# Optimization experiments

Hardware: AMD Instinct MI355X
Metric: run time of the kernel (lower is better)

The kernel has to match this reference:

```python
import jax, jax.numpy as jnp
import numpy as np

COUT, CIN = 1024, 1024  # self.shape = (cout, cin) in the torch module
NNZ = 131072


def setup_inputs() -> dict:
    key = jax.random.key(0)
    k_x, k_v, k_r, k_c = jax.random.split(key, 4)
    x = jax.random.normal(k_x, (4, 4096, CIN), dtype=jnp.float32)
    values = jax.random.normal(k_v, (NNZ,), dtype=jnp.float32)
    rows = jax.random.randint(k_r, (NNZ,), 0, COUT, dtype=jnp.int32)
    cols = jax.random.randint(k_c, (NNZ,), 0, CIN, dtype=jnp.int32)
    indices = jnp.stack([rows, cols], axis=0)  # [2, nnz], integer-valued
    return {"x": x, "values": values, "indices": indices}


def reference(x, values, indices):
    # torch: sparse_coo_tensor(indices, values, (cout, cin)).coalesce();
    # coalescing sums duplicate (row, col) entries -> scatter-add densify.
    rows, cols = indices[0], indices[1]
    W = jnp.zeros((COUT, CIN), dtype=values.dtype).at[rows, cols].add(values)
    # 3D path: out[b, l, co] = sum_ci W[co, ci] * x[b, l, ci]
    return jnp.einsum('blc,oc->blo', x, W)
```

## Files before the change

### kernel.cpp

```cpp
#include <hip/hip_runtime.h>
#include <cstdint>
#include <cstddef>

#define CIN  1024
#define COUT 1024

typedef __attribute__((ext_vector_type(8))) short bf16x8;
typedef __attribute__((ext_vector_type(4))) float f32x4;

__device__ __forceinline__ unsigned short f2bf(float f) {
    union { float f; unsigned int i; } v;
    v.f = f;
    unsigned int u = v.i;
    u += 0x7FFFu + ((u >> 16) & 1u);
    return (unsigned short)(u >> 16);
}

__global__ void zero_f32(float4* __restrict__ p) {
    p[blockIdx.x * 256 + threadIdx.x] = float4{0.f, 0.f, 0.f, 0.f};
}

__global__ void scatter_add(const float* __restrict__ vals,
                            const int* __restrict__ rows,
                            const int* __restrict__ cols,
                            float* __restrict__ W, int nnz) {
    int i = blockIdx.x * 256 + threadIdx.x;
    if (i < nnz) {
        atomicAdd(W + (size_t)rows[i] * CIN + cols[i], vals[i]);
    }
}

__global__ void cvt_bf16_bulk(const float* __restrict__ src, unsigned short* __restrict__ dst) {
    size_t i = ((size_t)blockIdx.x * 256 + threadIdx.x) * 8;
    float4 v0 = *(const float4*)(src + i);
    float4 v1 = *(const float4*)(src + i + 4);
    union { bf16x8 v; unsigned short u[8]; } w;
    w.u[0] = f2bf(v0.x); w.u[1] = f2bf(v0.y); w.u[2] = f2bf(v0.z); w.u[3] = f2bf(v0.w);
    w.u[4] = f2bf(v1.x); w.u[5] = f2bf(v1.y); w.u[6] = f2bf(v1.z); w.u[7] = f2bf(v1.w);
    *(bf16x8*)(dst + i) = w.v;
}

__global__ __launch_bounds__(256) void gemm_bt_bf16_sw(
    const unsigned short* __restrict__ A,
    const unsigned short* __restrict__ B,
    float* __restrict__ C,
    int M) {
    constexpr int K = CIN;
    constexpr int N = COUT;

    __shared__ __align__(16) unsigned short As[128 * 64];
    __shared__ __align__(16) unsigned short Bs[128 * 64];

    const int tid   = threadIdx.x;
    const int lane  = tid & 63;
    const int wave  = tid >> 6;
    const int waveM = (wave >> 1) * 64;
    const int waveN = (wave & 1) * 64;
    const int quad  = lane >> 4;
    const int l16   = lane & 15;

    const int rowA0 = blockIdx.x * 128;
    const int rowB0 = blockIdx.y * 128;

    const int stg_r  = tid >> 3;
    const int c_slot = tid & 7;
    const int c_data = c_slot ^ (stg_r & 7);
    const unsigned short* pa = A + (size_t)(rowA0 + stg_r) * K + c_data * 8;
    const unsigned short* pb = B + (size_t)(rowB0 + stg_r) * K + c_data * 8;
    const int ldsoff = tid * 8;

    f32x4 acc[4][4] = {};

    for (int k0 = 0; k0 < K; k0 += 64) {
#pragma unroll
        for (int it = 0; it < 4; ++it) {
            __builtin_amdgcn_global_load_lds(
                (const __attribute__((address_space(1))) void*)(pa + k0 + (size_t)it * 32 * K),
                (__attribute__((address_space(3))) void*)(As + it * 2048 + ldsoff),
                16, 0, 0);
            __builtin_amdgcn_global_load_lds(
                (const __attribute__((address_space(1))) void*)(pb + k0 + (size_t)it * 32 * K),
                (__attribute__((address_space(3))) void*)(Bs + it * 2048 + ldsoff),
                16, 0, 0);
        }
        __syncthreads();

        const int s7 = l16 & 7;
#pragma unroll
        for (int ks = 0; ks < 2; ++ks) {
            bf16x8 af[4], bfr[4];
            const int cx = ((ks * 4 + quad) ^ s7) * 8;
#pragma unroll
            for (int t = 0; t < 4; ++t) {
                af[t]  = *(const bf16x8*)(As + (waveM + t * 16 + l16) * 64 + cx);
                bfr[t] = *(const bf16x8*)(Bs + (waveN + t * 16 + l16) * 64 + cx);
            }
#pragma unroll
            for (int i = 0; i < 4; ++i)
#pragma unroll
                for (int j = 0; j < 4; ++j)
                    acc[i][j] = __builtin_amdgcn_mfma_f32_16x16x32_bf16(
                        af[i], bfr[j], acc[i][j], 0, 0, 0);
        }
        __syncthreads();
    }

#pragma unroll
    for (int i = 0; i < 4; ++i) {
#pragma unroll
        for (int r = 0; r < 4; ++r) {
            const int row = rowA0 + waveM + i * 16 + quad * 4 + r;
            float* cp = C + (size_t)row * N + rowB0 + waveN + l16;
#pragma unroll
            for (int j = 0; j < 4; ++j)
                cp[j * 16] = acc[i][j][r];
        }
    }
}

extern "C" void kernel_launch(void* const* d_in, const int* in_sizes, int n_in,
                              void* d_out, int out_size, void* d_ws, size_t ws_size,
                              hipStream_t stream) {
    const float* x    = (const float*)d_in[0];
    const float* vals = (const float*)d_in[1];
    const int*   idx  = (const int*)d_in[2];

    float* out = (float*)d_out;

    const int nnz = in_sizes[2] / 2;
    const int M   = in_sizes[0] / CIN;

    const size_t wf_bytes = (size_t)COUT * CIN * sizeof(float);
    const size_t wb_bytes = (size_t)COUT * CIN * sizeof(unsigned short);

    float*          Wf = (float*)d_ws;
    unsigned short* Wb = (unsigned short*)((char*)d_ws + wf_bytes);
    unsigned short* Xb = (unsigned short*)((char*)d_ws + wf_bytes + wb_bytes);

    zero_f32<<<dim3(COUT * CIN / (256 * 4)), dim3(256), 0, stream>>>((float4*)Wf);
    scatter_add<<<dim3((nnz + 255) / 256), dim3(256), 0, stream>>>(vals, idx, idx + nnz, Wf, nnz);
    cvt_bf16_bulk<<<dim3(COUT * CIN / (256 * 8)), dim3(256), 0, stream>>>(Wf, Wb);
    cvt_bf16_bulk<<<dim3((unsigned)((size_t)M * CIN / (256 * 8))), dim3(256), 0, stream>>>(x, Xb);
    gemm_bt_bf16_sw<<<dim3(M / 128, COUT / 128), dim3(256), 0, stream>>>(Xb, Wb, out, M);
}
```

Measured before the change: 163.8 us.

## Load A fragments directly from global memory and stage larger B tiles in LDS

The GEMM stops staging the activation tile in shared memory and has each lane read its bf16 A fragments straight from global memory. The weight tile is staged in LDS in 256-wide K chunks, which cuts the number of barrier-separated iterations from sixteen to four. The aim is to remove the A LDS traffic and the barrier overhead. In exchange it adds uncoalesced global loads, duplicate A reads across waves, and 64KB of LDS per block, which may lower occupancy.

```diff
diff --git a/kernel.cpp b/kernel.cpp
--- a/kernel.cpp
+++ b/kernel.cpp
@@ -40,7 +40,7 @@
     *(bf16x8*)(dst + i) = w.v;
 }
 
-__global__ __launch_bounds__(256) void gemm_bt_bf16_sw(
+__global__ __launch_bounds__(256) void gemm_adirect(
     const unsigned short* __restrict__ A,
     const unsigned short* __restrict__ B,
     float* __restrict__ C,
@@ -48,8 +48,7 @@
     constexpr int K = CIN;
     constexpr int N = COUT;
 
-    __shared__ __align__(16) unsigned short As[128 * 64];
-    __shared__ __align__(16) unsigned short Bs[128 * 64];
+    __shared__ __align__(16) unsigned short Bs[128 * 256];
 
     const int tid   = threadIdx.x;
     const int lane  = tid & 63;
@@ -62,47 +61,48 @@
     const int rowA0 = blockIdx.x * 128;
     const int rowB0 = blockIdx.y * 128;
 
-    const int stg_r  = tid >> 3;
-    const int c_slot = tid & 7;
-    const int c_data = c_slot ^ (stg_r & 7);
-    const unsigned short* pa = A + (size_t)(rowA0 + stg_r) * K + c_data * 8;
-    const unsigned short* pb = B + (size_t)(rowB0 + stg_r) * K + c_data * 8;
+    const int s_slot = tid & 31;
+    const int r_low  = tid >> 5;
+    const int c_data = (s_slot & ~7) | ((s_slot & 7) ^ r_low);
+    const unsigned short* pb = B + (size_t)(rowB0 + r_low) * K + c_data * 8;
     const int ldsoff = tid * 8;
 
+    const unsigned short* pa = A + (size_t)(rowA0 + waveM + l16) * K + quad * 8;
+
     f32x4 acc[4][4] = {};
+    const int s7 = l16 & 7;
 
-    for (int k0 = 0; k0 < K; k0 += 64) {
+    for (int kq = 0; kq < 4; ++kq) {
+        if (kq) __syncthreads();
 #pragma unroll
-        for (int it = 0; it < 4; ++it) {
+        for (int i = 0; i < 16; ++i) {
             __builtin_amdgcn_global_load_lds(
-                (const __attribute__((address_space(1))) void*)(pa + k0 + (size_t)it * 32 * K),
-                (__attribute__((address_space(3))) void*)(As + it * 2048 + ldsoff),
-                16, 0, 0);
-            __builtin_amdgcn_global_load_lds(
-                (const __attribute__((address_space(1))) void*)(pb + k0 + (size_t)it * 32 * K),
-                (__attribute__((address_space(3))) void*)(Bs + it * 2048 + ldsoff),
+                (const __attribute__((address_space(1))) void*)(pb + kq * 256 + (size_t)i * 8 * K),
+                (__attribute__((address_space(3))) void*)(Bs + i * 2048 + ldsoff),
                 16, 0, 0);
         }
         __syncthreads();
 
-        const int s7 = l16 & 7;
 #pragma unroll
-        for (int ks = 0; ks < 2; ++ks) {
-            bf16x8 af[4], bfr[4];
-            const int cx = ((ks * 4 + quad) ^ s7) * 8;
+        for (int sub = 0; sub < 4; ++sub) {
+            const int kbase = kq * 256 + sub * 64;
 #pragma unroll
-            for (int t = 0; t < 4; ++t) {
-                af[t]  = *(const bf16x8*)(As + (waveM + t * 16 + l16) * 64 + cx);
-                bfr[t] = *(const bf16x8*)(Bs + (waveN + t * 16 + l16) * 64 + cx);
+            for (int ks = 0; ks < 2; ++ks) {
+                bf16x8 af[4], bfr[4];
+                const int cx = sub * 64 + ((ks * 4 + quad) ^ s7) * 8;
+#pragma unroll
+                for (int t = 0; t < 4; ++t) {
+                    af[t]  = *(const bf16x8*)(pa + (size_t)t * 16 * K + kbase + ks * 32);
+                    bfr[t] = *(const bf16x8*)(Bs + (waveN + t * 16 + l16) * 256 + cx);
+                }
+#pragma unroll
+                for (int i = 0; i < 4; ++i)
+#pragma unroll
+                    for (int j = 0; j < 4; ++j)
+                        acc[i][j] = __builtin_amdgcn_mfma_f32_16x16x32_bf16(
+                            af[i], bfr[j], acc[i][j], 0, 0, 0);
             }
-#pragma unroll
-            for (int i = 0; i < 4; ++i)
-#pragma unroll
-                for (int j = 0; j < 4; ++j)
-                    acc[i][j] = __builtin_amdgcn_mfma_f32_16x16x32_bf16(
-                        af[i], bfr[j], acc[i][j], 0, 0, 0);
         }
-        __syncthreads();
     }
 
 #pragma unroll
@@ -141,5 +141,5 @@
     scatter_add<<<dim3((nnz + 255) / 256), dim3(256), 0, stream>>>(vals, idx, idx + nnz, Wf, nnz);
     cvt_bf16_bulk<<<dim3(COUT * CIN / (256 * 8)), dim3(256), 0, stream>>>(Wf, Wb);
     cvt_bf16_bulk<<<dim3((unsigned)((size_t)M * CIN / (256 * 8))), dim3(256), 0, stream>>>(x, Xb);
-    gemm_bt_bf16_sw<<<dim3(M / 128, COUT / 128), dim3(256), 0, stream>>>(Xb, Wb, out, M);
+    gemm_adirect<<<dim3(M / 128, COUT / 128), dim3(256), 0, stream>>>(Xb, Wb, out, M);
 }
```

New measurement: 194.5 us. +18.7%, slower.
